# Kernel optimization log

Hardware: AMD Instinct MI355X
Metric: run time of the kernel (lower is better)

## Reference

```python
import jax, jax.numpy as jnp
import numpy as np

N_QUBITS = 8
N_LAYERS = 4
DIM = 2 ** N_QUBITS  # 256 state-vector

# PauliZ sign table: signs[i, idx] = +1 if bit of wire i in basis index idx is 0 else -1.
# Wire 0 is the most-significant axis (state axes ordered wire0..wire{n-1}).
_idx = np.arange(DIM)
SIGNS = np.stack([1.0 - 2.0 * ((_idx >> (N_QUBITS - 1 - i)) & 1) for i in range(N_QUBITS)]).astype(np.float32)  # [n, 256]


def _rx_mat(theta):
    c = jnp.cos(0.5 * theta).astype(jnp.complex64)
    s = (-1j * jnp.sin(0.5 * theta)).astype(jnp.complex64)
    return jnp.stack([jnp.stack([c, s]), jnp.stack([s, c])])  # [2,2]


def _rz_diag(theta):
    return jnp.stack([jnp.exp(-0.5j * theta), jnp.exp(0.5j * theta)]).astype(jnp.complex64)  # [2]


def _apply_1q(state, U, w):
    # state: (2,)*n complex64; apply 2x2 U on wire w
    st = jnp.moveaxis(state, w, 0).reshape(2, -1)
    st = U @ st
    return jnp.moveaxis(st.reshape((2,) * N_QUBITS), 0, w)


def _apply_diag(state, d, w):
    st = jnp.moveaxis(state, w, 0)
    st = st * d.reshape((2,) + (1,) * (N_QUBITS - 1))
    return jnp.moveaxis(st, 0, w)


def _cnot(state, c, t):
    st = jnp.moveaxis(state, (c, t), (0, 1))
    st = jnp.stack([st[0], st[1][::-1]], axis=0)  # flip target where control==1
    return jnp.moveaxis(st, (0, 1), (c, t))


def _circuit(angles, weights):
    # angles: [n_qubits], weights: [n_layers, 2, n_qubits] -> expvals [n_qubits]
    state = jnp.zeros((2,) * N_QUBITS, jnp.complex64).at[(0,) * N_QUBITS].set(1.0)
    for i in range(N_QUBITS):
        state = _apply_1q(state, _rx_mat(angles[i]), i)
        state = _apply_diag(state, _rz_diag(angles[i]), i)
    for l in range(N_LAYERS):
        for i in range(N_QUBITS):
            state = _apply_1q(state, _rx_mat(weights[l, 0, i]), i)
            state = _apply_diag(state, _rz_diag(weights[l, 1, i]), i)
        for i in range(N_QUBITS - 1):
            state = _cnot(state, i, i + 1)
    probs = jnp.abs(state.reshape(-1)) ** 2  # [256]
    return (probs @ SIGNS.T).astype(jnp.float32)  # [n_qubits] <Z_i>


def setup_inputs() -> dict:
    key = jax.random.key(0)
    B, D_IN, D_OUT = 8192, 1024, 1024
    ks = jax.random.split(key, 6)
    bound_in = np.sqrt(6.0 / D_IN)  # kaiming_uniform fan_in, linear
    bound_out = np.sqrt(6.0 / N_QUBITS)
    return {
        "x": jax.random.normal(ks[0], (B, D_IN), jnp.float32),
        "W_in": jax.random.uniform(ks[1], (N_QUBITS, D_IN), jnp.float32, -bound_in, bound_in),
        "b_in": jnp.zeros((N_QUBITS,), jnp.float32),
        "q_weights": jax.random.uniform(ks[2], (N_LAYERS, 2, N_QUBITS), jnp.float32, 0.0, 2.0 * np.pi),
        "W_out": jax.random.uniform(ks[3], (D_OUT, N_QUBITS), jnp.float32, -bound_out, bound_out),
        "b_out": jnp.zeros((D_OUT,), jnp.float32),
    }


def reference(x, W_in, b_in, q_weights, W_out, b_out):
    x_proj = x @ W_in.T + b_in                                   # [B, n_qubits]
    ev = jax.vmap(_circuit, in_axes=(0, None))(x_proj, q_weights)  # [B, n_qubits]
    return ev @ W_out.T + b_out                                   # [B, output_dim]
```

## Files before the change

kernel.cpp:

```cpp
#include <hip/hip_runtime.h>
#include <math.h>


typedef float f32x2 __attribute__((ext_vector_type(2)));

__device__ __forceinline__ int f2i(float v) { return __float_as_int(v); }
__device__ __forceinline__ float i2f(int v) { return __int_as_float(v); }

template <int CTRL>
__device__ __forceinline__ float dppf(float v) {
    return i2f(__builtin_amdgcn_update_dpp(0, f2i(v), CTRL, 0xF, 0xF, true));
}

template <int ML>
__device__ __forceinline__ float gshm(float v) {
    static_assert(ML > 0 && ML < 64, "lane mask");
    if constexpr (ML == 1)      return dppf<0xB1>(v);
    else if constexpr (ML == 2) return dppf<0x4E>(v);
    else if constexpr (ML == 3) return dppf<0x1B>(v);
    else if constexpr (ML == 8) return dppf<0x128>(v);
    else if constexpr (ML < 32) return i2f(__builtin_amdgcn_ds_swizzle(f2i(v), 0x1F | (ML << 10)));
    else                        return __shfl_xor(v, ML, 64);
}

template <int L>
__device__ __forceinline__ float rdlane(float v) {
    return i2f(__builtin_amdgcn_readlane(f2i(v), L));
}

template <int ML, int MR, int ZL, int ZR>
__device__ __forceinline__ void ggate(f32x2& reA, f32x2& reB, f32x2& imA, f32x2& imB,
                                      float c1, float s1, float c2, float s2,
                                      int lane) {
    f32x2 sReA, sReB, sImA, sImB;
    if constexpr (MR == 0)      { sReA = reA;    sReB = reB;    sImA = imA;    sImB = imB; }
    else if constexpr (MR == 1) { sReA = reA.yx; sReB = reB.yx; sImA = imA.yx; sImB = imB.yx; }
    else if constexpr (MR == 2) { sReA = reB;    sReB = reA;    sImA = imB;    sImB = imA; }
    else                        { sReA = reB.yx; sReB = reA.yx; sImA = imB.yx; sImB = imA.yx; }
    f32x2 pReA, pReB, pImA, pImB;
    if constexpr (ML != 0) {
        pReA.x = gshm<ML>(sReA.x); pReA.y = gshm<ML>(sReA.y);
        pReB.x = gshm<ML>(sReB.x); pReB.y = gshm<ML>(sReB.y);
        pImA.x = gshm<ML>(sImA.x); pImA.y = gshm<ML>(sImA.y);
        pImB.x = gshm<ML>(sImB.x); pImB.y = gshm<ML>(sImB.y);
    } else { pReA = sReA; pReB = sReB; pImA = sImA; pImB = sImB; }
    f32x2 nReA = c1 * reA + s1 * pImA;
    f32x2 nReB = c1 * reB + s1 * pImB;
    f32x2 nImA = c1 * imA - s1 * pReA;
    f32x2 nImB = c1 * imB - s1 * pReB;
    float base;
    if constexpr (ZL == 0) base = -s2;
    else                   base = (__popc(lane & ZL) & 1) ? s2 : -s2;
    constexpr bool N1 = (ZR & 1) != 0;
    constexpr bool N2 = ((ZR >> 1) & 1) != 0;
    constexpr bool N3 = (((ZR & 1) ^ ((ZR >> 1) & 1)) != 0);
    f32x2 ssA = { base, N1 ? -base : base };
    f32x2 ssB = { N2 ? -base : base, N3 ? -base : base };
    f32x2 tA = c2 * nReA - ssA * nImA;
    f32x2 tB = c2 * nReB - ssB * nImB;
    imA = c2 * nImA + ssA * nReA;
    imB = c2 * nImB + ssB * nReB;
    reA = tA;
    reB = tB;
}

template <int BASE>
__device__ __forceinline__ void expand_state(float ur2, float ui2, float vr2, float vi2,
                                             int lane,
                                             f32x2& reA, f32x2& reB, f32x2& imA, f32x2& imB) {
    float Pr, Pi;
    {
        float fur = rdlane<BASE + 0>(ur2), fui = rdlane<BASE + 0>(ui2);
        float fvr = rdlane<BASE + 0>(vr2), fvi = rdlane<BASE + 0>(vi2);
        bool b = (lane >> 5) & 1;
        Pr = b ? fvr : fur;
        Pi = b ? fvi : fui;
    }
#define PMUL(W_, L_) { \
        float fur = rdlane<BASE + L_>(ur2), fui = rdlane<BASE + L_>(ui2); \
        float fvr = rdlane<BASE + L_>(vr2), fvi = rdlane<BASE + L_>(vi2); \
        bool b = (lane >> (5 - (W_))) & 1; \
        float fr = b ? fvr : fur, fi = b ? fvi : fui; \
        float tr = Pr * fr - Pi * fi; \
        Pi = Pr * fi + Pi * fr; \
        Pr = tr; }
    PMUL(1, 1) PMUL(2, 2) PMUL(3, 3) PMUL(4, 8) PMUL(5, 9)
#undef PMUL
    {
        float u6r = rdlane<BASE + 10>(ur2), u6i = rdlane<BASE + 10>(ui2);
        float v6r = rdlane<BASE + 10>(vr2), v6i = rdlane<BASE + 10>(vi2);
        float u7r = rdlane<BASE + 11>(ur2), u7i = rdlane<BASE + 11>(ui2);
        float v7r = rdlane<BASE + 11>(vr2), v7i = rdlane<BASE + 11>(vi2);
        float rr[4], ii[4];
#pragma unroll
        for (int r = 0; r < 4; ++r) {
            float g6r_ = (r & 2) ? v6r : u6r, g6i_ = (r & 2) ? v6i : u6i;
            float g7r_ = (r & 1) ? v7r : u7r, g7i_ = (r & 1) ? v7i : u7i;
            float fr = g6r_ * g7r_ - g6i_ * g7i_;
            float fi = g6r_ * g7i_ + g6i_ * g7r_;
            rr[r] = Pr * fr - Pi * fi;
            ii[r] = Pr * fi + Pi * fr;
        }
        reA = (f32x2){ rr[0], rr[1] };  reB = (f32x2){ rr[2], rr[3] };
        imA = (f32x2){ ii[0], ii[1] };  imB = (f32x2){ ii[2], ii[3] };
    }
}

__global__ void __launch_bounds__(256, 4) qasa_kernel(
    const float* __restrict__ x, const float* __restrict__ W_in,
    const float* __restrict__ b_in, const float* __restrict__ qw,
    const float* __restrict__ W_out, const float* __restrict__ b_out,
    float* __restrict__ out)
{
    const int tid = threadIdx.x;
    const int lane = tid & 63;
    const int w = tid >> 6;
    const int block8 = blockIdx.x * 8;

    __shared__ float ang[64];
    __shared__ float evs[8][8] __attribute__((aligned(16)));

    float vc, vs;
    __sincosf(0.5f * qw[lane], &vs, &vc);

    const int b0 = lane & 1, b1 = (lane >> 1) & 1, b3 = (lane >> 3) & 1;
    const int qofl = b0 | (b1 << 1) | (b3 << 2);
    const float binq = b_in[qofl];

    {
        const float4* w4 = (const float4*)W_in;
        float4 wv0[4], wv1[4];
#pragma unroll
        for (int k = 0; k < 4; ++k) {
            wv0[k] = w4[(2 * w) * 256 + lane + 64 * k];
            wv1[k] = w4[(2 * w + 1) * 256 + lane + 64 * k];
        }
        const float4* xr0 = (const float4*)(x + (size_t)block8 * 1024);
        const float4* xr1 = (const float4*)(x + (size_t)(block8 + 4) * 1024);

        float4 xv[4][4];
#pragma unroll
        for (int r = 0; r < 4; ++r)
#pragma unroll
            for (int k = 0; k < 4; ++k)
                xv[r][k] = xr0[r * 256 + lane + 64 * k];

        f32x2 acc2[8];
#pragma unroll
        for (int j = 0; j < 8; ++j) acc2[j] = (f32x2){0.f, 0.f};
#pragma unroll
        for (int k = 0; k < 4; ++k)
#pragma unroll
            for (int r = 0; r < 4; ++r) {
                float4 xvv = xv[r][k];
                acc2[r]     += (f32x2){xvv.x, xvv.y} * (f32x2){wv0[k].x, wv0[k].y}
                             + (f32x2){xvv.z, xvv.w} * (f32x2){wv0[k].z, wv0[k].w};
                acc2[4 + r] += (f32x2){xvv.x, xvv.y} * (f32x2){wv1[k].x, wv1[k].y}
                             + (f32x2){xvv.z, xvv.w} * (f32x2){wv1[k].z, wv1[k].w};
            }

        float4 yv[4][4];
#pragma unroll
        for (int r = 0; r < 4; ++r)
#pragma unroll
            for (int k = 0; k < 4; ++k)
                yv[r][k] = xr1[r * 256 + lane + 64 * k];

        {
            float acc[8];
#pragma unroll
            for (int j = 0; j < 8; ++j) {
                acc[j] = acc2[j].x + acc2[j].y;
                acc[j] += dppf<0xB1>(acc[j]);
                acc[j] += dppf<0x4E>(acc[j]);
                acc[j] += dppf<0x128>(acc[j]);
            }
            float t01 = b0 ? acc[1] : acc[0];
            float t23 = b0 ? acc[3] : acc[2];
            float t45 = b0 ? acc[5] : acc[4];
            float t67 = b0 ? acc[7] : acc[6];
            float ta = b1 ? t23 : t01;
            float tb = b1 ? t67 : t45;
            float S = b3 ? tb : ta;
            S += gshm<4>(S); S += gshm<16>(S); S += gshm<32>(S);
            if ((lane & 52) == 0)
                ang[(2 * w + ((lane >> 3) & 1)) * 8 + (lane & 3)] = S;
        }

        {
            f32x2 bcc2[8];
#pragma unroll
            for (int j = 0; j < 8; ++j) bcc2[j] = (f32x2){0.f, 0.f};
#pragma unroll
            for (int k = 0; k < 4; ++k)
#pragma unroll
                for (int r = 0; r < 4; ++r) {
                    float4 xvv = yv[r][k];
                    bcc2[r]     += (f32x2){xvv.x, xvv.y} * (f32x2){wv0[k].x, wv0[k].y}
                                 + (f32x2){xvv.z, xvv.w} * (f32x2){wv0[k].z, wv0[k].w};
                    bcc2[4 + r] += (f32x2){xvv.x, xvv.y} * (f32x2){wv1[k].x, wv1[k].y}
                                 + (f32x2){xvv.z, xvv.w} * (f32x2){wv1[k].z, wv1[k].w};
                }
            float acc[8];
#pragma unroll
            for (int j = 0; j < 8; ++j) {
                acc[j] = bcc2[j].x + bcc2[j].y;
                acc[j] += dppf<0xB1>(acc[j]);
                acc[j] += dppf<0x4E>(acc[j]);
                acc[j] += dppf<0x128>(acc[j]);
            }
            float t01 = b0 ? acc[1] : acc[0];
            float t23 = b0 ? acc[3] : acc[2];
            float t45 = b0 ? acc[5] : acc[4];
            float t67 = b0 ? acc[7] : acc[6];
            float ta = b1 ? t23 : t01;
            float tb = b1 ? t67 : t45;
            float S = b3 ? tb : ta;
            S += gshm<4>(S); S += gshm<16>(S); S += gshm<32>(S);
            if ((lane & 52) == 0)
                ang[(2 * w + ((lane >> 3) & 1)) * 8 + 4 + (lane & 3)] = S;
        }
    }
    __syncthreads();

    const int c4 = (w << 6) + lane;
    const float4* wo = (const float4*)W_out;
    float4 wa[4], wb[4];
#pragma unroll
    for (int c = 0; c < 4; ++c) {
        wa[c] = wo[2 * (4 * c4 + c)];
        wb[c] = wo[2 * (4 * c4 + c) + 1];
    }
    float4 bias = ((const float4*)b_out)[c4];

    const int rsel = w + ((lane >> 2) & 4);
    float A = ang[qofl * 8 + rsel] + binq;
    float ca, sa;
    __sincosf(0.5f * A, &sa, &ca);
    float ur = ca * ca, ui = -ca * sa, vr = sa * sa, vi = ui;
    const int a1 = 4 * qofl, a2 = 4 * (qofl + 8);
    float cx = i2f(__builtin_amdgcn_ds_bpermute(a1, f2i(vc)));
    float sx = i2f(__builtin_amdgcn_ds_bpermute(a1, f2i(vs)));
    float cz = i2f(__builtin_amdgcn_ds_bpermute(a2, f2i(vc)));
    float sz = i2f(__builtin_amdgcn_ds_bpermute(a2, f2i(vs)));
    float ur1 = cx * ur + sx * vi, ui1 = cx * ui - sx * vr;
    float vr1 = cx * vr + sx * ui, vi1 = cx * vi - sx * ur;
    float ur2 = cz * ur1 + sz * ui1, ui2 = cz * ui1 - sz * ur1;
    float vr2 = cz * vr1 - sz * vi1, vi2 = cz * vi1 + sz * vr1;

    f32x2 reA0, reB0, imA0, imB0;
    f32x2 reA1, reB1, imA1, imB1;
    expand_state<0>(ur2, ui2, vr2, vi2, lane, reA0, reB0, imA0, imB0);
    expand_state<16>(ur2, ui2, vr2, vi2, lane, reA1, reB1, imA1, imB1);

#define GG(Lx, W_, ML_, MR_, ZL_, ZR_) { \
    float c1 = rdlane<16 * (Lx) + (W_)>(vc), s1 = rdlane<16 * (Lx) + (W_)>(vs); \
    float c2 = rdlane<16 * (Lx) + 8 + (W_)>(vc), s2 = rdlane<16 * (Lx) + 8 + (W_)>(vs); \
    ggate<ML_, MR_, ZL_, ZR_>(reA0, reB0, imA0, imB0, c1, s1, c2, s2, lane); \
    ggate<ML_, MR_, ZL_, ZR_>(reA1, reB1, imA1, imB1, c1, s1, c2, s2, lane); }

    GG(1,0, 48,0, 32,0)  GG(1,1, 24,0, 48,0)  GG(1,2, 12,0, 56,0) GG(1,3, 6,0, 60,0)
    GG(1,4, 3,0, 62,0)   GG(1,5, 1,2, 63,0)   GG(1,6, 0,3, 63,2)  GG(1,7, 0,1, 63,3)
    GG(2,0, 40,0, 32,0)  GG(2,1, 20,0, 16,0)  GG(2,2, 10,0, 40,0) GG(2,3, 5,0, 20,0)
    GG(2,4, 2,2, 42,0)   GG(2,5, 1,1, 21,0)   GG(2,6, 0,2, 42,2)  GG(2,7, 0,1, 21,1)
    GG(3,0, 60,0, 32,0)  GG(3,1, 30,0, 48,0)  GG(3,2, 15,0, 24,0) GG(3,3, 7,2, 12,0)
    GG(3,4, 3,3, 38,0)   GG(3,5, 1,3, 51,0)   GG(3,6, 0,3, 25,2)  GG(3,7, 0,1, 12,3)
#undef GG

#define BUTTERFLY(reA, reB, imA, imB, vq0, vq1, vq2) \
    float p0 = reA.x * reA.x + imA.x * imA.x; \
    float p1 = reA.y * reA.y + imA.y * imA.y; \
    float p2 = reB.x * reB.x + imB.x * imB.x; \
    float p3 = reB.y * reB.y + imB.y * imB.y; \
    float vq0 = (p0 + p1) + (p2 + p3); \
    float vq2 = (p0 + p1) - (p2 + p3); \
    float vq1 = (p0 + p2) - (p1 + p3); \
    { float u = dppf<0xB1>(vq0);  vq0 = (lane & 1)  ? (u - vq0) : (vq0 + u); } \
    { float u = dppf<0x4E>(vq0);  vq0 = (lane & 2)  ? (u - vq0) : (vq0 + u); } \
    { float u = dppf<0x128>(vq0); vq0 = (lane & 8)  ? (u - vq0) : (vq0 + u); } \
    { float u = gshm<4>(vq0);     vq0 = (lane & 4)  ? (u - vq0) : (vq0 + u); } \
    { float u = gshm<16>(vq0);    vq0 = (lane & 16) ? (u - vq0) : (vq0 + u); } \
    { float u = gshm<32>(vq0);    vq0 = (lane & 32) ? (u - vq0) : (vq0 + u); } \
    vq2 += dppf<0xB1>(vq2); \
    vq2 += dppf<0x4E>(vq2); \
    { float u = dppf<0x128>(vq2); vq2 = (lane & 8) ? (u - vq2) : (vq2 + u); } \
    vq2 += gshm<4>(vq2); vq2 += gshm<16>(vq2); vq2 += gshm<32>(vq2); \
    vq1 += dppf<0xB1>(vq1); \
    vq1 += dppf<0x4E>(vq1); \
    vq1 += dppf<0x128>(vq1); \
    { float u = gshm<4>(vq1); vq1 = (lane & 4) ? (u - vq1) : (vq1 + u); } \
    vq1 += gshm<16>(vq1); vq1 += gshm<32>(vq1);

    float v0, v1, q1A, q1B, q2A, q2B;
    { BUTTERFLY(reA0, reB0, imA0, imB0, vv, w1, w2) v0 = vv; q1A = w1; q2A = w2; }
    { BUTTERFLY(reA1, reB1, imA1, imB1, vv, w1, w2) v1 = vv; q1B = w1; q2B = w2; }
#undef BUTTERFLY

    {
        const unsigned long long wrmask = 0x0000000500030110ULL;
        if ((wrmask >> lane) & 1) {
            int k = 6 - __ffs(lane);
            evs[w][k] = v0;
            evs[w + 4][k] = v1;
        }
        if (lane == 8) { evs[w][6] = q2A; evs[w + 4][6] = q2B; }
        if (lane == 4) { evs[w][7] = q1A; evs[w + 4][7] = q1B; }
    }
    __syncthreads();

    {
#pragma unroll
        for (int r = 0; r < 8; ++r) {
            const float4* ev4 = (const float4*)evs[r];
            float4 lo = ev4[0], hi = ev4[1];
            f32x2 E01 = { lo.x, lo.y }, E23 = { lo.z, lo.w };
            f32x2 E45 = { hi.x, hi.y }, E67 = { hi.z, hi.w };
            float res[4];
#pragma unroll
            for (int c = 0; c < 4; ++c) {
                f32x2 a2 = E01 * (f32x2){ wa[c].x, wa[c].y } + E23 * (f32x2){ wa[c].z, wa[c].w }
                         + E45 * (f32x2){ wb[c].x, wb[c].y } + E67 * (f32x2){ wb[c].z, wb[c].w };
                res[c] = a2.x + a2.y;
            }
            float4 o;
            o.x = bias.x + res[0]; o.y = bias.y + res[1];
            o.z = bias.z + res[2]; o.w = bias.w + res[3];
            ((float4*)(out + (size_t)(block8 + r) * 1024))[c4] = o;
        }
    }
}

extern "C" void kernel_launch(void* const* d_in, const int* in_sizes, int n_in,
                              void* d_out, int out_size, void* d_ws, size_t ws_size,
                              hipStream_t stream) {
    const float* x     = (const float*)d_in[0];
    const float* W_in  = (const float*)d_in[1];
    const float* b_in  = (const float*)d_in[2];
    const float* qw    = (const float*)d_in[3];
    const float* W_out = (const float*)d_in[4];
    const float* b_out = (const float*)d_in[5];
    float* outp = (float*)d_out;

    const int B = in_sizes[0] / 1024;
    const int grid = B / 8;
    qasa_kernel<<<grid, 256, 0, stream>>>(x, W_in, b_in, qw, W_out, b_out, outp);
}
```

Measured before the change: 103.7 us.

## Remap state-vector layout to 8 amplitudes per lane over 32-lane halves

Changes the state-vector distribution from two 4-amplitude batch samples per lane across 64 lanes to one sample per 32-lane half, each lane holding 8 amplitudes. Gate application is rewritten for 8 register amplitudes, with new cross-lane masks that use DPP row operations for masks 7 and 15 where possible. The per-sample expansion now uses ds_bpermute instead of readlane. The final PauliZ butterfly reductions are restructured to match the new layout. The aim is fewer cross-lane shuffles and readlanes per gate, paid for with more registers and LDS bpermute traffic.

```diff
diff --git a/kernel.cpp b/kernel.cpp
--- a/kernel.cpp
+++ b/kernel.cpp
@@ -15,12 +15,14 @@
 template <int ML>
 __device__ __forceinline__ float gshm(float v) {
     static_assert(ML > 0 && ML < 64, "lane mask");
-    if constexpr (ML == 1)      return dppf<0xB1>(v);
-    else if constexpr (ML == 2) return dppf<0x4E>(v);
-    else if constexpr (ML == 3) return dppf<0x1B>(v);
-    else if constexpr (ML == 8) return dppf<0x128>(v);
-    else if constexpr (ML < 32) return i2f(__builtin_amdgcn_ds_swizzle(f2i(v), 0x1F | (ML << 10)));
-    else                        return __shfl_xor(v, ML, 64);
+    if constexpr (ML == 1)       return dppf<0xB1>(v);
+    else if constexpr (ML == 2)  return dppf<0x4E>(v);
+    else if constexpr (ML == 3)  return dppf<0x1B>(v);
+    else if constexpr (ML == 7)  return dppf<0x141>(v);
+    else if constexpr (ML == 8)  return dppf<0x128>(v);
+    else if constexpr (ML == 15) return dppf<0x140>(v);
+    else if constexpr (ML < 32)  return i2f(__builtin_amdgcn_ds_swizzle(f2i(v), 0x1F | (ML << 10)));
+    else                         return __shfl_xor(v, 32, 64);
 }
 
 template <int L>
@@ -28,81 +30,39 @@
     return i2f(__builtin_amdgcn_readlane(f2i(v), L));
 }
 
+__device__ __forceinline__ float bpermf(int addr, float v) {
+    return i2f(__builtin_amdgcn_ds_bpermute(addr, f2i(v)));
+}
+
 template <int ML, int MR, int ZL, int ZR>
-__device__ __forceinline__ void ggate(f32x2& reA, f32x2& reB, f32x2& imA, f32x2& imB,
-                                      float c1, float s1, float c2, float s2,
-                                      int lane) {
-    f32x2 sReA, sReB, sImA, sImB;
-    if constexpr (MR == 0)      { sReA = reA;    sReB = reB;    sImA = imA;    sImB = imB; }
-    else if constexpr (MR == 1) { sReA = reA.yx; sReB = reB.yx; sImA = imA.yx; sImB = imB.yx; }
-    else if constexpr (MR == 2) { sReA = reB;    sReB = reA;    sImA = imB;    sImB = imA; }
-    else                        { sReA = reB.yx; sReB = reA.yx; sImA = imB.yx; sImB = imA.yx; }
-    f32x2 pReA, pReB, pImA, pImB;
-    if constexpr (ML != 0) {
-        pReA.x = gshm<ML>(sReA.x); pReA.y = gshm<ML>(sReA.y);
-        pReB.x = gshm<ML>(sReB.x); pReB.y = gshm<ML>(sReB.y);
-        pImA.x = gshm<ML>(sImA.x); pImA.y = gshm<ML>(sImA.y);
-        pImB.x = gshm<ML>(sImB.x); pImB.y = gshm<ML>(sImB.y);
-    } else { pReA = sReA; pReB = sReB; pImA = sImA; pImB = sImB; }
-    f32x2 nReA = c1 * reA + s1 * pImA;
-    f32x2 nReB = c1 * reB + s1 * pImB;
-    f32x2 nImA = c1 * imA - s1 * pReA;
-    f32x2 nImB = c1 * imB - s1 * pReB;
+__device__ __forceinline__ void ggate8(f32x2 re[4], f32x2 im[4],
+                                       float c1, float s1, float c2, float s2,
+                                       int lane) {
+    constexpr int JM = MR >> 1;
+    constexpr bool CM = (MR & 1) != 0;
+    f32x2 pRe[4], pIm[4];
+#pragma unroll
+    for (int j = 0; j < 4; ++j) {
+        f32x2 sR = re[j ^ JM], sI = im[j ^ JM];
+        if constexpr (CM) { sR = sR.yx; sI = sI.yx; }
+        if constexpr (ML != 0) {
+            pRe[j].x = gshm<ML>(sR.x); pRe[j].y = gshm<ML>(sR.y);
+            pIm[j].x = gshm<ML>(sI.x); pIm[j].y = gshm<ML>(sI.y);
+        } else { pRe[j] = sR; pIm[j] = sI; }
+    }
     float base;
     if constexpr (ZL == 0) base = -s2;
     else                   base = (__popc(lane & ZL) & 1) ? s2 : -s2;
-    constexpr bool N1 = (ZR & 1) != 0;
-    constexpr bool N2 = ((ZR >> 1) & 1) != 0;
-    constexpr bool N3 = (((ZR & 1) ^ ((ZR >> 1) & 1)) != 0);
-    f32x2 ssA = { base, N1 ? -base : base };
-    f32x2 ssB = { N2 ? -base : base, N3 ? -base : base };
-    f32x2 tA = c2 * nReA - ssA * nImA;
-    f32x2 tB = c2 * nReB - ssB * nImB;
-    imA = c2 * nImA + ssA * nReA;
-    imB = c2 * nImB + ssB * nReB;
-    reA = tA;
-    reB = tB;
-}
-
-template <int BASE>
-__device__ __forceinline__ void expand_state(float ur2, float ui2, float vr2, float vi2,
-                                             int lane,
-                                             f32x2& reA, f32x2& reB, f32x2& imA, f32x2& imB) {
-    float Pr, Pi;
-    {
-        float fur = rdlane<BASE + 0>(ur2), fui = rdlane<BASE + 0>(ui2);
-        float fvr = rdlane<BASE + 0>(vr2), fvi = rdlane<BASE + 0>(vi2);
-        bool b = (lane >> 5) & 1;
-        Pr = b ? fvr : fur;
-        Pi = b ? fvi : fui;
-    }
-#define PMUL(W_, L_) { \
-        float fur = rdlane<BASE + L_>(ur2), fui = rdlane<BASE + L_>(ui2); \
-        float fvr = rdlane<BASE + L_>(vr2), fvi = rdlane<BASE + L_>(vi2); \
-        bool b = (lane >> (5 - (W_))) & 1; \
-        float fr = b ? fvr : fur, fi = b ? fvi : fui; \
-        float tr = Pr * fr - Pi * fi; \
-        Pi = Pr * fi + Pi * fr; \
-        Pr = tr; }
-    PMUL(1, 1) PMUL(2, 2) PMUL(3, 3) PMUL(4, 8) PMUL(5, 9)
-#undef PMUL
-    {
-        float u6r = rdlane<BASE + 10>(ur2), u6i = rdlane<BASE + 10>(ui2);
-        float v6r = rdlane<BASE + 10>(vr2), v6i = rdlane<BASE + 10>(vi2);
-        float u7r = rdlane<BASE + 11>(ur2), u7i = rdlane<BASE + 11>(ui2);
-        float v7r = rdlane<BASE + 11>(vr2), v7i = rdlane<BASE + 11>(vi2);
-        float rr[4], ii[4];
-#pragma unroll
-        for (int r = 0; r < 4; ++r) {
-            float g6r_ = (r & 2) ? v6r : u6r, g6i_ = (r & 2) ? v6i : u6i;
-            float g7r_ = (r & 1) ? v7r : u7r, g7i_ = (r & 1) ? v7i : u7i;
-            float fr = g6r_ * g7r_ - g6i_ * g7i_;
-            float fi = g6r_ * g7i_ + g6i_ * g7r_;
-            rr[r] = Pr * fr - Pi * fi;
-            ii[r] = Pr * fi + Pi * fr;
-        }
-        reA = (f32x2){ rr[0], rr[1] };  reB = (f32x2){ rr[2], rr[3] };
-        imA = (f32x2){ ii[0], ii[1] };  imB = (f32x2){ ii[2], ii[3] };
+#pragma unroll
+    for (int j = 0; j < 4; ++j) {
+        f32x2 nR = c1 * re[j] + s1 * pIm[j];
+        f32x2 nI = c1 * im[j] - s1 * pRe[j];
+        const int pj = __builtin_popcount(j & (ZR >> 1)) & 1;
+        float sj = pj ? -base : base;
+        float sc = (ZR & 1) ? -sj : sj;
+        f32x2 ss = { sj, sc };
+        re[j] = c2 * nR - ss * nI;
+        im[j] = c2 * nI + ss * nR;
     }
 }
 
@@ -186,7 +146,6 @@
             if ((lane & 52) == 0)
                 ang[(2 * w + ((lane >> 3) & 1)) * 8 + (lane & 3)] = S;
         }
-
         {
             f32x2 bcc2[8];
 #pragma unroll
@@ -233,78 +192,120 @@
     }
     float4 bias = ((const float4*)b_out)[c4];
 
-    const int rsel = w + ((lane >> 2) & 4);
-    float A = ang[qofl * 8 + rsel] + binq;
+    const int half32 = lane & 32;
+    const int rowsel = w + ((lane >> 3) & 4);
+    const int isV = (lane >> 4) & 1;
+    float A = ang[qofl * 8 + rowsel] + binq;
     float ca, sa;
     __sincosf(0.5f * A, &sa, &ca);
     float ur = ca * ca, ui = -ca * sa, vr = sa * sa, vi = ui;
     const int a1 = 4 * qofl, a2 = 4 * (qofl + 8);
-    float cx = i2f(__builtin_amdgcn_ds_bpermute(a1, f2i(vc)));
-    float sx = i2f(__builtin_amdgcn_ds_bpermute(a1, f2i(vs)));
-    float cz = i2f(__builtin_amdgcn_ds_bpermute(a2, f2i(vc)));
-    float sz = i2f(__builtin_amdgcn_ds_bpermute(a2, f2i(vs)));
+    float cx = bpermf(a1, vc);
+    float sx = bpermf(a1, vs);
+    float cz = bpermf(a2, vc);
+    float sz = bpermf(a2, vs);
     float ur1 = cx * ur + sx * vi, ui1 = cx * ui - sx * vr;
     float vr1 = cx * vr + sx * ui, vi1 = cx * vi - sx * ur;
     float ur2 = cz * ur1 + sz * ui1, ui2 = cz * ui1 - sz * ur1;
     float vr2 = cz * vr1 - sz * vi1, vi2 = cz * vi1 + sz * vr1;
-
-    f32x2 reA0, reB0, imA0, imB0;
-    f32x2 reA1, reB1, imA1, imB1;
-    expand_state<0>(ur2, ui2, vr2, vi2, lane, reA0, reB0, imA0, imB0);
-    expand_state<16>(ur2, ui2, vr2, vi2, lane, reA1, reB1, imA1, imB1);
+    const float fre = isV ? vr2 : ur2;
+    const float fim = isV ? vi2 : ui2;
+
+    float Pr, Pi;
+    {
+        int b = (lane >> 4) & 1;
+        int a = (half32 | (b << 4)) << 2;
+        Pr = bpermf(a, fre); Pi = bpermf(a, fim);
+    }
+#define PM(L_, SH_) { \
+        int b = (lane >> (SH_)) & 1; \
+        int a = (half32 + (L_) + (b << 4)) << 2; \
+        float fr = bpermf(a, fre), fi = bpermf(a, fim); \
+        float tr = Pr * fr - Pi * fi; \
+        Pi = Pr * fi + Pi * fr; Pr = tr; }
+    PM(1, 3) PM(2, 2) PM(3, 1) PM(8, 0)
+#undef PM
+    f32x2 re[4], im[4];
+    {
+        int a5u = (half32 + 9) << 2,  a5v = (half32 + 25) << 2;
+        int a6u = (half32 + 10) << 2, a6v = (half32 + 26) << 2;
+        int a7u = (half32 + 11) << 2, a7v = (half32 + 27) << 2;
+        float u5r = bpermf(a5u, fre), u5i = bpermf(a5u, fim);
+        float v5r = bpermf(a5v, fre), v5i = bpermf(a5v, fim);
+        float u6r = bpermf(a6u, fre), u6i = bpermf(a6u, fim);
+        float v6r = bpermf(a6v, fre), v6i = bpermf(a6v, fim);
+        float u7r = bpermf(a7u, fre), u7i = bpermf(a7u, fim);
+        float v7r = bpermf(a7v, fre), v7i = bpermf(a7v, fim);
+        float hr[4], hi[4];
+        hr[0] = u6r * u7r - u6i * u7i;  hi[0] = u6r * u7i + u6i * u7r;
+        hr[1] = u6r * v7r - u6i * v7i;  hi[1] = u6r * v7i + u6i * v7r;
+        hr[2] = v6r * u7r - v6i * u7i;  hi[2] = v6r * u7i + v6i * u7r;
+        hr[3] = v6r * v7r - v6i * v7i;  hi[3] = v6r * v7i + v6i * v7r;
+        float rr[8], ii[8];
+#pragma unroll
+        for (int r = 0; r < 8; ++r) {
+            float f5r = (r & 4) ? v5r : u5r, f5i = (r & 4) ? v5i : u5i;
+            float gr = f5r * hr[r & 3] - f5i * hi[r & 3];
+            float gi = f5r * hi[r & 3] + f5i * hr[r & 3];
+            rr[r] = Pr * gr - Pi * gi;
+            ii[r] = Pr * gi + Pi * gr;
+        }
+#pragma unroll
+        for (int j = 0; j < 4; ++j) {
+            re[j] = (f32x2){ rr[2 * j], rr[2 * j + 1] };
+            im[j] = (f32x2){ ii[2 * j], ii[2 * j + 1] };
+        }
+    }
 
 #define GG(Lx, W_, ML_, MR_, ZL_, ZR_) { \
     float c1 = rdlane<16 * (Lx) + (W_)>(vc), s1 = rdlane<16 * (Lx) + (W_)>(vs); \
     float c2 = rdlane<16 * (Lx) + 8 + (W_)>(vc), s2 = rdlane<16 * (Lx) + 8 + (W_)>(vs); \
-    ggate<ML_, MR_, ZL_, ZR_>(reA0, reB0, imA0, imB0, c1, s1, c2, s2, lane); \
-    ggate<ML_, MR_, ZL_, ZR_>(reA1, reB1, imA1, imB1, c1, s1, c2, s2, lane); }
-
-    GG(1,0, 48,0, 32,0)  GG(1,1, 24,0, 48,0)  GG(1,2, 12,0, 56,0) GG(1,3, 6,0, 60,0)
-    GG(1,4, 3,0, 62,0)   GG(1,5, 1,2, 63,0)   GG(1,6, 0,3, 63,2)  GG(1,7, 0,1, 63,3)
-    GG(2,0, 40,0, 32,0)  GG(2,1, 20,0, 16,0)  GG(2,2, 10,0, 40,0) GG(2,3, 5,0, 20,0)
-    GG(2,4, 2,2, 42,0)   GG(2,5, 1,1, 21,0)   GG(2,6, 0,2, 42,2)  GG(2,7, 0,1, 21,1)
-    GG(3,0, 60,0, 32,0)  GG(3,1, 30,0, 48,0)  GG(3,2, 15,0, 24,0) GG(3,3, 7,2, 12,0)
-    GG(3,4, 3,3, 38,0)   GG(3,5, 1,3, 51,0)   GG(3,6, 0,3, 25,2)  GG(3,7, 0,1, 12,3)
+    ggate8<ML_, MR_, ZL_, ZR_>(re, im, c1, s1, c2, s2, lane); }
+
+    GG(1,0, 24,0, 16,0)  GG(1,1, 12,0, 24,0)  GG(1,2, 6,0, 28,0)  GG(1,3, 3,0, 30,0)
+    GG(1,4, 1,4, 31,0)   GG(1,5, 0,6, 31,4)   GG(1,6, 0,3, 31,6)  GG(1,7, 0,1, 31,7)
+    GG(2,0, 20,0, 16,0)  GG(2,1, 10,0, 8,0)   GG(2,2, 5,0, 20,0)  GG(2,3, 2,4, 10,0)
+    GG(2,4, 1,2, 21,0)   GG(2,5, 0,5, 10,4)   GG(2,6, 0,2, 21,2)  GG(2,7, 0,1, 10,5)
+    GG(3,0, 30,0, 16,0)  GG(3,1, 15,0, 24,0)  GG(3,2, 7,4, 12,0)  GG(3,3, 3,6, 6,0)
+    GG(3,4, 1,7, 19,0)   GG(3,5, 0,7, 25,4)   GG(3,6, 0,3, 12,6)  GG(3,7, 0,1, 6,3)
 #undef GG
 
-#define BUTTERFLY(reA, reB, imA, imB, vq0, vq1, vq2) \
-    float p0 = reA.x * reA.x + imA.x * imA.x; \
-    float p1 = reA.y * reA.y + imA.y * imA.y; \
-    float p2 = reB.x * reB.x + imB.x * imB.x; \
-    float p3 = reB.y * reB.y + imB.y * imB.y; \
-    float vq0 = (p0 + p1) + (p2 + p3); \
-    float vq2 = (p0 + p1) - (p2 + p3); \
-    float vq1 = (p0 + p2) - (p1 + p3); \
-    { float u = dppf<0xB1>(vq0);  vq0 = (lane & 1)  ? (u - vq0) : (vq0 + u); } \
-    { float u = dppf<0x4E>(vq0);  vq0 = (lane & 2)  ? (u - vq0) : (vq0 + u); } \
-    { float u = dppf<0x128>(vq0); vq0 = (lane & 8)  ? (u - vq0) : (vq0 + u); } \
-    { float u = gshm<4>(vq0);     vq0 = (lane & 4)  ? (u - vq0) : (vq0 + u); } \
-    { float u = gshm<16>(vq0);    vq0 = (lane & 16) ? (u - vq0) : (vq0 + u); } \
-    { float u = gshm<32>(vq0);    vq0 = (lane & 32) ? (u - vq0) : (vq0 + u); } \
-    vq2 += dppf<0xB1>(vq2); \
-    vq2 += dppf<0x4E>(vq2); \
-    { float u = dppf<0x128>(vq2); vq2 = (lane & 8) ? (u - vq2) : (vq2 + u); } \
-    vq2 += gshm<4>(vq2); vq2 += gshm<16>(vq2); vq2 += gshm<32>(vq2); \
-    vq1 += dppf<0xB1>(vq1); \
-    vq1 += dppf<0x4E>(vq1); \
-    vq1 += dppf<0x128>(vq1); \
-    { float u = gshm<4>(vq1); vq1 = (lane & 4) ? (u - vq1) : (vq1 + u); } \
-    vq1 += gshm<16>(vq1); vq1 += gshm<32>(vq1);
-
-    float v0, v1, q1A, q1B, q2A, q2B;
-    { BUTTERFLY(reA0, reB0, imA0, imB0, vv, w1, w2) v0 = vv; q1A = w1; q2A = w2; }
-    { BUTTERFLY(reA1, reB1, imA1, imB1, vv, w1, w2) v1 = vv; q1B = w1; q2B = w2; }
-#undef BUTTERFLY
-
-    {
-        const unsigned long long wrmask = 0x0000000500030110ULL;
-        if ((wrmask >> lane) & 1) {
-            int k = 6 - __ffs(lane);
-            evs[w][k] = v0;
-            evs[w + 4][k] = v1;
-        }
-        if (lane == 8) { evs[w][6] = q2A; evs[w + 4][6] = q2B; }
-        if (lane == 4) { evs[w][7] = q1A; evs[w + 4][7] = q1B; }
+    {
+        f32x2 pp0 = re[0] * re[0] + im[0] * im[0];
+        f32x2 pp1 = re[1] * re[1] + im[1] * im[1];
+        f32x2 pp2 = re[2] * re[2] + im[2] * im[2];
+        f32x2 pp3 = re[3] * re[3] + im[3] * im[3];
+        float sx0 = pp0.x + pp0.y, dx0 = pp0.x - pp0.y;
+        float sx1 = pp1.x + pp1.y, dx1 = pp1.x - pp1.y;
+        float sx2 = pp2.x + pp2.y, dx2 = pp2.x - pp2.y;
+        float sx3 = pp3.x + pp3.y, dx3 = pp3.x - pp3.y;
+        float q0 = (sx0 + sx1) + (sx2 + sx3);
+        float q1 = (dx0 + dx1) + (dx2 + dx3);
+        float q2 = (sx0 - sx1) + (sx2 - sx3);
+        float q4 = (sx0 + sx1) - (sx2 + sx3);
+
+        { float u = dppf<0xB1>(q0);  q0 = (lane & 1)  ? (u - q0) : (q0 + u); }
+        { float u = dppf<0x4E>(q0);  q0 = (lane & 2)  ? (u - q0) : (q0 + u); }
+        { float u = gshm<4>(q0);     q0 = (lane & 4)  ? (u - q0) : (q0 + u); }
+        { float u = dppf<0x128>(q0); q0 = (lane & 8)  ? (u - q0) : (q0 + u); }
+        { float u = gshm<16>(q0);    q0 = (lane & 16) ? (u - q0) : (q0 + u); }
+        q4 += dppf<0xB1>(q4); q4 += dppf<0x4E>(q4); q4 += gshm<4>(q4);
+        { float u = dppf<0x128>(q4); q4 = (lane & 8) ? (u - q4) : (q4 + u); }
+        q4 += gshm<16>(q4);
+        q2 += dppf<0xB1>(q2); q2 += dppf<0x4E>(q2);
+        { float u = gshm<4>(q2); q2 = (lane & 4) ? (u - q2) : (q2 + u); }
+        q2 += dppf<0x128>(q2); q2 += gshm<16>(q2);
+        q1 += dppf<0xB1>(q1);
+        { float u = dppf<0x4E>(q1); q1 = (lane & 2) ? (u - q1) : (q1 + u); }
+        q1 += gshm<4>(q1); q1 += dppf<0x128>(q1); q1 += gshm<16>(q1);
+
+        const int l5 = lane & 31;
+        const int row = rowsel;
+        if (l5 == 16)      { evs[row][0] = q0; }
+        else if (l5 == 8)  { evs[row][1] = q0; evs[row][5] = q4; }
+        else if (l5 == 4)  { evs[row][2] = q0; evs[row][6] = q2; }
+        else if (l5 == 2)  { evs[row][3] = q0; evs[row][7] = q1; }
+        else if (l5 == 17) { evs[row][4] = q0; }
     }
     __syncthreads();
 
@@ -318,9 +319,9 @@
             float res[4];
 #pragma unroll
             for (int c = 0; c < 4; ++c) {
-                f32x2 a2 = E01 * (f32x2){ wa[c].x, wa[c].y } + E23 * (f32x2){ wa[c].z, wa[c].w }
-                         + E45 * (f32x2){ wb[c].x, wb[c].y } + E67 * (f32x2){ wb[c].z, wb[c].w };
-                res[c] = a2.x + a2.y;
+                f32x2 a2v = E01 * (f32x2){ wa[c].x, wa[c].y } + E23 * (f32x2){ wa[c].z, wa[c].w }
+                          + E45 * (f32x2){ wb[c].x, wb[c].y } + E67 * (f32x2){ wb[c].z, wb[c].w };
+                res[c] = a2v.x + a2v.y;
             }
             float4 o;
             o.x = bias.x + res[0]; o.y = bias.y + res[1];
```

Result: no change. 102.5 us (-1.2%).
